# Kernel tuning notes

Hardware: AMD Instinct MI355X
Metric: run time of the kernel (lower is better)

## Reference

```python
import jax, jax.numpy as jnp
import numpy as np
import math

D_MODEL = 1024
N_HEADS = 16
RANK = 256  # int(d_model * 0.25)
RANK_PER_HEAD = RANK // N_HEADS  # 16
HEAD_DIM = D_MODEL // N_HEADS  # 64
B, L = 32, 512


def setup_inputs() -> dict:
    key = jax.random.key(0)
    kx, kq, kk, kv, ku, kvv = jax.random.split(key, 6)
    x = jax.random.normal(kx, (B, L, D_MODEL), dtype=jnp.float32)
    mask = jnp.ones((B, L), dtype=bool)
    s = 1.0 / math.sqrt(D_MODEL)
    Wq = jax.random.normal(kq, (RANK, D_MODEL), dtype=jnp.float32) * s
    Wk = jax.random.normal(kk, (RANK, D_MODEL), dtype=jnp.float32) * s
    Wv = jax.random.normal(kv, (RANK, D_MODEL), dtype=jnp.float32) * s
    # xavier_uniform for U [H, head_dim, r_h] and V [H, r_h, head_dim]
    lim = math.sqrt(6.0 / (HEAD_DIM + RANK_PER_HEAD))
    U = jax.random.uniform(ku, (N_HEADS, HEAD_DIM, RANK_PER_HEAD), jnp.float32, -lim, lim)
    V = jax.random.uniform(kvv, (N_HEADS, RANK_PER_HEAD, HEAD_DIM), jnp.float32, -lim, lim)
    return {"x": x, "mask": mask, "Wq": Wq, "Wk": Wk, "Wv": Wv, "U": U, "V": V}


def _rope_tables(seq_len, head_dim, dtype):
    half = head_dim // 2
    theta = 1.0 / (10000.0 ** (jnp.arange(half, dtype=jnp.float32) / half))
    freqs = jnp.arange(seq_len, dtype=jnp.float32)[:, None] * theta[None, :]  # [L, half]
    return jnp.cos(freqs).astype(dtype), jnp.sin(freqs).astype(dtype)


def _apply_rope(x, cos, sin):
    # x: [B, L, H, D]; complex multiply on interleaved pairs
    Bq, Lq, H, D = x.shape
    xr = x.reshape(Bq, Lq, H, D // 2, 2)
    x0, x1 = xr[..., 0], xr[..., 1]
    c = cos[None, :, None, :]
    s = sin[None, :, None, :]
    o0 = x0 * c - x1 * s
    o1 = x0 * s + x1 * c
    return jnp.stack([o0, o1], axis=-1).reshape(Bq, Lq, H, D)


def reference(x, mask, Wq, Wk, Wv, U, V):
    Bq, Lq, _ = x.shape
    H, head_dim, r_h = U.shape
    q_low = (x @ Wq.T).reshape(Bq, Lq, H, r_h)
    k_low = (x @ Wk.T).reshape(Bq, Lq, H, r_h)
    v_low = (x @ Wv.T).reshape(Bq, Lq, H, r_h)
    q = jnp.einsum('hdr,blhr->blhd', U, q_low)
    k = jnp.einsum('hdr,blhr->blhd', U, k_low)
    cos, sin = _rope_tables(Lq, head_dim, x.dtype)
    q = _apply_rope(q, cos, sin)
    k = _apply_rope(k, cos, sin)
    attn = jnp.einsum('blhd,bmhd->bhlm', q, k) / math.sqrt(head_dim)
    attn = jnp.where(mask[:, None, None, :], attn, -jnp.inf)
    attn = jax.nn.softmax(attn, axis=-1)
    out = jnp.einsum('bhlm,bmhr->blhr', attn, v_low)
    out = jnp.einsum('blhr,hrd->blhd', out, V)
    return out.reshape(Bq, Lq, H * head_dim)
```

## Files before the change

kernel.cpp:

```cpp
#include <hip/hip_runtime.h>
#include <hip/hip_bf16.h>

#define B_   32
#define L_   512
#define DM_  1024
#define H_   16
#define RH_  16
#define HD_  64
#define NTOK (B_ * L_)

typedef short s16x8 __attribute__((ext_vector_type(8)));
typedef float f32x4 __attribute__((ext_vector_type(4)));
#define MFMA16(a,b,c) __builtin_amdgcn_mfma_f32_16x16x32_bf16(a, b, c, 0, 0, 0)

#define GLOAD_LDS16(g, l) __builtin_amdgcn_global_load_lds( \
    (const __attribute__((address_space(1))) unsigned int*)(g), \
    (__attribute__((address_space(3))) unsigned int*)(l), 16, 0, 0)

#if __has_builtin(__builtin_amdgcn_exp2f)
#define EXP2N(x) __builtin_amdgcn_exp2f(x)
#else
#define EXP2N(x) __expf((x) * 0.69314718055994531f)
#endif

__device__ inline ushort f2bf(float f) {
    unsigned u = __builtin_bit_cast(unsigned, f);
    u += 0x7fffu + ((u >> 16) & 1u);
    return (ushort)(u >> 16);
}
__device__ inline float bf2f(ushort u) {
    return __builtin_bit_cast(float, (unsigned)u << 16);
}

__global__ __launch_bounds__(256) void cvt_w(const float* __restrict__ Wq,
                                             const float* __restrict__ Wk,
                                             const float* __restrict__ Wv,
                                             ushort* __restrict__ dst) {
    const size_t i = ((size_t)blockIdx.x * 256 + threadIdx.x) * 8;
    const size_t sz = 256 * 1024;
    const float* src = (i < sz) ? (Wq + i) : (i < 2 * sz) ? (Wk + i - sz)
                                                          : (Wv + i - 2 * sz);
    float4 a = *(const float4*)(src);
    float4 b = *(const float4*)(src + 4);
    ushort o[8] = {f2bf(a.x), f2bf(a.y), f2bf(a.z), f2bf(a.w),
                   f2bf(b.x), f2bf(b.y), f2bf(b.z), f2bf(b.w)};
    *(uint4*)(dst + i) = *(const uint4*)o;
}

__global__ __launch_bounds__(256) void proj_mfma(
    const float*  __restrict__ X,
    const ushort* __restrict__ Bm,
    float* __restrict__ C)
{
    const int gid = blockIdx.x;
    const int g48 = gid / 48;
    const int rr  = gid - g48 * 48;
    const int bn  = rr >> 3;
    const int bm  = g48 * 8 + (rr & 7);
    const int tid = threadIdx.x;
    const int lane = tid & 63;
    const int ln15 = lane & 15, quad = lane >> 4;
    const int w = tid >> 6, wy = w >> 1, wx = w & 1;

    __shared__ ushort As[128 * 64];
    __shared__ ushort Bs[2][128 * 64];

    const int srow = tid >> 3;
    const int gch  = (tid & 7) ^ (srow & 7);
    const float*  Ag = X  + ((size_t)(bm * 128 + srow)) * DM_ + gch * 8;
    const ushort* Bg = Bm + ((size_t)(bn * 128 + srow)) * DM_ + gch * 8;
    ushort* Al = As + tid * 8;

    f32x4 acc[4][4] = {};
    float4 pa0[4], pa1[4];

    #pragma unroll
    for (int i = 0; i < 4; ++i)
        GLOAD_LDS16(Bg + (size_t)(i * 32) * DM_, &Bs[0][tid * 8 + i * 2048]);
    __builtin_amdgcn_sched_barrier(0);
    #pragma unroll
    for (int i = 0; i < 4; ++i) {
        pa0[i] = *(const float4*)(Ag + (size_t)(i * 32) * DM_);
        pa1[i] = *(const float4*)(Ag + (size_t)(i * 32) * DM_ + 4);
    }

    for (int kt = 0; kt < DM_ / 64; ++kt) {
        const int cur = kt & 1;
        __builtin_amdgcn_sched_barrier(0);
        __builtin_amdgcn_s_barrier();
        __builtin_amdgcn_sched_barrier(0);

        #pragma unroll
        for (int i = 0; i < 4; ++i) {
            ushort o[8] = {f2bf(pa0[i].x), f2bf(pa0[i].y), f2bf(pa0[i].z), f2bf(pa0[i].w),
                           f2bf(pa1[i].x), f2bf(pa1[i].y), f2bf(pa1[i].z), f2bf(pa1[i].w)};
            *(uint4*)(Al + i * 2048) = *(const uint4*)o;
        }
        if (kt < DM_ / 64 - 1) {
            const size_t ko = (size_t)(kt + 1) * 64;
            ushort* Bln = &Bs[cur ^ 1][tid * 8];
            #pragma unroll
            for (int i = 0; i < 4; ++i)
                GLOAD_LDS16(Bg + (size_t)(i * 32) * DM_ + ko, Bln + i * 2048);
            __builtin_amdgcn_sched_barrier(0);
            #pragma unroll
            for (int i = 0; i < 4; ++i) {
                pa0[i] = *(const float4*)(Ag + (size_t)(i * 32) * DM_ + ko);
                pa1[i] = *(const float4*)(Ag + (size_t)(i * 32) * DM_ + ko + 4);
            }
        }
        asm volatile("s_waitcnt lgkmcnt(0)" ::: "memory");
        __builtin_amdgcn_sched_barrier(0);
        __builtin_amdgcn_s_barrier();
        __builtin_amdgcn_sched_barrier(0);

        const ushort* Bcur = Bs[cur];
        s16x8 Af[4][2], Bf[4][2];
        #pragma unroll
        for (int i = 0; i < 4; ++i) {
            const int m = wy * 64 + i * 16 + ln15;
            const int n = wx * 64 + i * 16 + ln15;
            #pragma unroll
            for (int kh = 0; kh < 2; ++kh) {
                const int c = kh * 4 + quad;
                Af[i][kh] = *(const s16x8*)&As[m * 64 + ((c ^ (m & 7)) * 8)];
                Bf[i][kh] = *(const s16x8*)&Bcur[n * 64 + ((c ^ (n & 7)) * 8)];
            }
        }
        #pragma unroll
        for (int i = 0; i < 4; ++i)
            #pragma unroll
            for (int j = 0; j < 4; ++j) {
                acc[i][j] = MFMA16(Af[i][0], Bf[j][0], acc[i][j]);
                acc[i][j] = MFMA16(Af[i][1], Bf[j][1], acc[i][j]);
            }
    }

    #pragma unroll
    for (int i = 0; i < 4; ++i) {
        #pragma unroll
        for (int r = 0; r < 4; ++r) {
            const int grow = bm * 128 + wy * 64 + i * 16 + quad * 4 + r;
            float* cp = C + (size_t)grow * 768 + bn * 128 + wx * 64 + ln15;
            #pragma unroll
            for (int j = 0; j < 4; ++j)
                cp[j * 16] = acc[i][j][r];
        }
    }
}

#define USTRIDE 1032
#define VSTRIDE 520

__global__ __launch_bounds__(512) void expand_rope(
    const float* __restrict__ low,
    const float* __restrict__ U,
    ushort* __restrict__ qr,
    ushort* __restrict__ kr,
    ushort* __restrict__ vt)
{
    const int blk = blockIdx.x;
    const int b   = blk >> 4;
    const int l0  = (blk & 15) * 32;
    const int tid = threadIdx.x;
    const int h   = tid >> 5;
    const int tok = tid & 31;
    const int l   = l0 + tok;
    const int t   = b * L_ + l;

    __shared__ ushort Uls[16 * USTRIDE];
    __shared__ ushort vst[16 * VSTRIDE];

    float ql[16], kl[16], vl[16];
    {
        const float* lp = low + (size_t)t * 768 + h * 16;
        #pragma unroll
        for (int j = 0; j < 4; ++j) {
            float4 a = *(const float4*)(lp + j * 4);
            float4 c = *(const float4*)(lp + 256 + j * 4);
            float4 v = *(const float4*)(lp + 512 + j * 4);
            ql[j*4+0]=a.x; ql[j*4+1]=a.y; ql[j*4+2]=a.z; ql[j*4+3]=a.w;
            kl[j*4+0]=c.x; kl[j*4+1]=c.y; kl[j*4+2]=c.z; kl[j*4+3]=c.w;
            vl[j*4+0]=v.x; vl[j*4+1]=v.y; vl[j*4+2]=v.z; vl[j*4+3]=v.w;
        }
    }

    #pragma unroll
    for (int k = 0; k < 8; ++k) {
        const int e4 = tid + k * 512;
        float4 u4 = ((const float4*)U)[e4];
        const int g = e4 * 4;
        const int hh = g >> 10, off = g & 1023;
        ushort o[4] = {f2bf(u4.x), f2bf(u4.y), f2bf(u4.z), f2bf(u4.w)};
        *(ushort4*)&Uls[hh * USTRIDE + off] = *(const ushort4*)o;
    }
    __syncthreads();

    #pragma unroll
    for (int r = 0; r < 16; ++r)
        vst[h * VSTRIDE + r * 32 + tok] = f2bf(vl[r]);

    const ushort* Uh = &Uls[h * USTRIDE];
    const size_t bh8 = (size_t)(b * H_ + h) * 8;
    ushort* qp = qr + (bh8 * L_ + (size_t)l) * 8;
    ushort* kp = kr + (bh8 * L_ + (size_t)l) * 8;
    const float L2C = 13.287712379549449f / 32.0f;
    const float QSCALE = 0.18033688011112042f;

    #pragma unroll
    for (int ch = 0; ch < 8; ++ch) {
        float qv[8], kv[8];
        #pragma unroll
        for (int d = 0; d < 8; ++d) {
            const int dd = ch * 8 + d;
            s16x8 u0 = *(const s16x8*)&Uh[dd * 16];
            s16x8 u1 = *(const s16x8*)&Uh[dd * 16 + 8];
            float s1 = 0.f, s2 = 0.f;
            #pragma unroll
            for (int r = 0; r < 8; ++r) {
                const float uf = bf2f((ushort)u0[r]);
                s1 = fmaf(uf, ql[r], s1);
                s2 = fmaf(uf, kl[r], s2);
            }
            #pragma unroll
            for (int r = 0; r < 8; ++r) {
                const float uf = bf2f((ushort)u1[r]);
                s1 = fmaf(uf, ql[8 + r], s1);
                s2 = fmaf(uf, kl[8 + r], s2);
            }
            qv[d] = s1; kv[d] = s2;
        }
        #pragma unroll
        for (int pj = 0; pj < 4; ++pj) {
            const int i = ch * 4 + pj;
            const float ang = (float)l * exp2f(-(float)i * L2C);
            const float c = __cosf(ang), s = __sinf(ang);
            float x0 = qv[2*pj], x1 = qv[2*pj+1];
            qv[2*pj]   = x0 * c - x1 * s;
            qv[2*pj+1] = x0 * s + x1 * c;
            x0 = kv[2*pj]; x1 = kv[2*pj+1];
            kv[2*pj]   = x0 * c - x1 * s;
            kv[2*pj+1] = x0 * s + x1 * c;
        }
        ushort qo[8], ko[8];
        #pragma unroll
        for (int d = 0; d < 8; ++d) {
            qo[d] = f2bf(qv[d] * QSCALE);
            ko[d] = f2bf(kv[d]);
        }
        *(uint4*)(qp + (size_t)ch * L_ * 8) = *(const uint4*)qo;
        *(uint4*)(kp + (size_t)ch * L_ * 8) = *(const uint4*)ko;
    }

    __syncthreads();

    #pragma unroll
    for (int k = 0; k < 2; ++k) {
        const int c = tid + k * 512;
        const int hh = c >> 6, rr = (c >> 2) & 15, j = c & 3;
        uint4 v = *(const uint4*)&vst[hh * VSTRIDE + rr * 32 + j * 8];
        *(uint4*)&vt[(((size_t)(b * H_ + hh) * RH_) + rr) * L_ + l0 + j * 8] = v;
    }
}

__global__ __launch_bounds__(512) void attn_mfma(
    const ushort* __restrict__ qr,
    const ushort* __restrict__ kr,
    const ushort* __restrict__ vt,
    const float*  __restrict__ V,
    float* __restrict__ out)
{
    const int gid = blockIdx.x;
    const int bh = ((gid >> 5) << 3) | (gid & 7);
    const int qt = (gid >> 3) & 3;
    const int b = bh >> 4, h = bh & 15;
    const int tid = threadIdx.x;
    const int w = tid >> 6, lane = tid & 63;
    const int ln15 = lane & 15, quad = lane >> 4;

    __shared__ ushort Ks[2][64 * 64];
    __shared__ ushort Vts[2][16 * 64];
    __shared__ ushort Pb[8][16 * 64];
    __shared__ float  VhS[16 * 64];

    if (tid < 256)
        *(float4*)&VhS[tid * 4] = *(const float4*)(V + (size_t)h * RH_ * HD_ + tid * 4);

    const int qrow = qt * 128 + w * 16 + ln15;
    const size_t bh8 = (size_t)bh * 8;
    s16x8 Qf0 = *(const s16x8*)(qr + ((bh8 + quad) * L_ + qrow) * 8);
    s16x8 Qf1 = *(const s16x8*)(qr + ((bh8 + 4 + quad) * L_ + qrow) * 8);

    const ushort* kbase = kr + bh8 * L_ * 8;
    const ushort* vbase = vt + (size_t)bh * RH_ * L_;

    float lsum = 0.f;
    f32x4 Oacc = {0.f, 0.f, 0.f, 0.f};

    auto stage = [&](int c, int buf) {
        {
            const int key = tid >> 3, ch = tid & 7;
            const int chS = ch ^ (key & 7);
            GLOAD_LDS16(kbase + ((size_t)chS * L_ + c * 64 + key) * 8,
                        &Ks[buf][tid * 8]);
        }
        if (w < 2) {
            const int r = tid >> 3, ch = tid & 7;
            GLOAD_LDS16(vbase + (size_t)r * L_ + c * 64 + ((ch ^ (r & 7)) * 8),
                        &Vts[buf][tid * 8]);
        }
    };

    stage(0, 0);
    __syncthreads();

    for (int c = 0; c < 8; ++c) {
        const int cur = c & 1;
        if (c < 7) stage(c + 1, cur ^ 1);

        f32x4 Sc[4];
        #pragma unroll
        for (int ct = 0; ct < 4; ++ct) {
            const int key = ln15 + 16 * ct;
            s16x8 k0 = *(const s16x8*)&Ks[cur][key * 64 + ((quad ^ (key & 7)) * 8)];
            s16x8 k1 = *(const s16x8*)&Ks[cur][key * 64 + (((4 + quad) ^ (key & 7)) * 8)];
            f32x4 acc = {0.f, 0.f, 0.f, 0.f};
            acc = MFMA16(k0, Qf0, acc);
            acc = MFMA16(k1, Qf1, acc);
            Sc[ct] = acc;
        }

        ushort* pb = Pb[w];
        float tsum = 0.f;
        #pragma unroll
        for (int ct = 0; ct < 4; ++ct) {
            const float p0 = EXP2N(Sc[ct][0]);
            const float p1 = EXP2N(Sc[ct][1]);
            const float p2 = EXP2N(Sc[ct][2]);
            const float p3 = EXP2N(Sc[ct][3]);
            tsum += (p0 + p1) + (p2 + p3);
            uint2 pk;
            pk.x = (unsigned)f2bf(p0) | ((unsigned)f2bf(p1) << 16);
            pk.y = (unsigned)f2bf(p2) | ((unsigned)f2bf(p3) << 16);
            const int key0 = ct * 16 + quad * 4;
            const int chp = key0 >> 3, kop = key0 & 7;
            *(uint2*)&pb[ln15 * 64 + ((chp ^ (ln15 & 7)) * 8) + kop] = pk;
        }
        lsum += tsum;

        asm volatile("s_waitcnt lgkmcnt(0)" ::: "memory");
        __builtin_amdgcn_sched_barrier(0);

        #pragma unroll
        for (int half = 0; half < 2; ++half) {
            const int ch = half * 4 + quad;
            s16x8 pa = *(const s16x8*)&pb[ln15 * 64 + ((ch ^ (ln15 & 7)) * 8)];
            s16x8 vb = *(const s16x8*)&Vts[cur][ln15 * 64 + ((ch ^ (ln15 & 7)) * 8)];
            Oacc = MFMA16(pa, vb, Oacc);
        }

        __syncthreads();
    }

    lsum += __shfl_xor(lsum, 16, 64);
    lsum += __shfl_xor(lsum, 32, 64);
    const float inv = 1.0f / lsum;

    float* Olds = (float*)Pb[w];
    #pragma unroll
    for (int r = 0; r < 4; ++r) {
        const float li = __shfl(inv, quad * 4 + r, 64);
        Olds[(quad * 4 + r) * 16 + ln15] = Oacc[r] * li;
    }
    asm volatile("s_waitcnt lgkmcnt(0)" ::: "memory");
    __builtin_amdgcn_sched_barrier(0);

    const int q = lane >> 2, dc = lane & 3;
    float orow[16];
    #pragma unroll
    for (int j = 0; j < 4; ++j) {
        float4 o4 = *(const float4*)&Olds[q * 16 + j * 4];
        orow[j * 4 + 0] = o4.x; orow[j * 4 + 1] = o4.y;
        orow[j * 4 + 2] = o4.z; orow[j * 4 + 3] = o4.w;
    }
    float4 res[4] = {};
    #pragma unroll
    for (int r = 0; r < 16; ++r) {
        const float ov = orow[r];
        #pragma unroll
        for (int j = 0; j < 4; ++j) {
            float4 v4 = *(const float4*)&VhS[r * 64 + dc * 16 + j * 4];
            res[j].x = fmaf(ov, v4.x, res[j].x);
            res[j].y = fmaf(ov, v4.y, res[j].y);
            res[j].z = fmaf(ov, v4.z, res[j].z);
            res[j].w = fmaf(ov, v4.w, res[j].w);
        }
    }
    const int l = qt * 128 + w * 16 + q;
    float* op = out + (((size_t)b * L_ + l) * H_ + h) * HD_ + dc * 16;
    #pragma unroll
    for (int j = 0; j < 4; ++j)
        *(float4*)(op + j * 4) = res[j];
}

extern "C" void kernel_launch(void* const* d_in, const int* in_sizes, int n_in,
                              void* d_out, int out_size, void* d_ws, size_t ws_size,
                              hipStream_t stream) {
    const float* x  = (const float*)d_in[0];
    const float* Wq = (const float*)d_in[2];
    const float* Wk = (const float*)d_in[3];
    const float* Wv = (const float*)d_in[4];
    const float* U  = (const float*)d_in[5];
    const float* V  = (const float*)d_in[6];
    float* out = (float*)d_out;

    float*  low = (float*)d_ws;
    ushort* Wb  = (ushort*)(low + (size_t)NTOK * 768);
    ushort* vtb = Wb + (size_t)768 * DM_;
    ushort* qrb = vtb + (size_t)B_ * H_ * RH_ * L_;
    ushort* krb = qrb + (size_t)B_ * H_ * L_ * HD_;

    cvt_w<<<768 * DM_ / (256 * 8), 256, 0, stream>>>(Wq, Wk, Wv, Wb);
    proj_mfma<<<768, 256, 0, stream>>>(x, Wb, low);
    expand_rope<<<512, 512, 0, stream>>>(low, U, qrb, krb, vtb);
    attn_mfma<<<B_ * H_ * 4, 512, 0, stream>>>(qrb, krb, vtb, V, out);
}
```

Measured before the change: 257.4 us.

## Split expand_rope work across head groups and output halves to raise occupancy

Restructures the expand_rope kernel from 512 blocks of 512 threads (one thread per token-head computing all 64 dims for q and k) into 2048 blocks of 256 threads. Each block now covers 4 heads, and each thread computes half the head dimensions, doing q and k one after the other. This cuts per-thread register pressure and shared-memory footprint (U staging is only 4 heads) and adds launch_bounds(256,5), aiming for more parallelism and better latency hiding. The cost is that each thread reloads its low-rank inputs and recomputes the rope angles, and the v transpose is done by half the threads.

```diff
diff --git a/kernel.cpp b/kernel.cpp
--- a/kernel.cpp
+++ b/kernel.cpp
@@ -149,10 +149,7 @@
     }
 }
 
-#define USTRIDE 1032
-#define VSTRIDE 520
-
-__global__ __launch_bounds__(512) void expand_rope(
+__global__ __launch_bounds__(256, 5) void expand_rope(
     const float* __restrict__ low,
     const float* __restrict__ U,
     ushort* __restrict__ qr,
@@ -160,106 +157,99 @@
     ushort* __restrict__ vt)
 {
     const int blk = blockIdx.x;
-    const int b   = blk >> 4;
-    const int l0  = (blk & 15) * 32;
+    const int b   = blk >> 6;
+    const int sub = blk & 63;
+    const int l0  = (sub >> 2) * 32;
+    const int hg  = sub & 3;
     const int tid = threadIdx.x;
-    const int h   = tid >> 5;
     const int tok = tid & 31;
+    const int h2  = (tid >> 5) & 3;
+    const int dh  = tid >> 7;
+    const int h   = hg * 4 + h2;
     const int l   = l0 + tok;
     const int t   = b * L_ + l;
 
-    __shared__ ushort Uls[16 * USTRIDE];
-    __shared__ ushort vst[16 * VSTRIDE];
-
-    float ql[16], kl[16], vl[16];
-    {
-        const float* lp = low + (size_t)t * 768 + h * 16;
-        #pragma unroll
-        for (int j = 0; j < 4; ++j) {
-            float4 a = *(const float4*)(lp + j * 4);
-            float4 c = *(const float4*)(lp + 256 + j * 4);
-            float4 v = *(const float4*)(lp + 512 + j * 4);
-            ql[j*4+0]=a.x; ql[j*4+1]=a.y; ql[j*4+2]=a.z; ql[j*4+3]=a.w;
-            kl[j*4+0]=c.x; kl[j*4+1]=c.y; kl[j*4+2]=c.z; kl[j*4+3]=c.w;
-            vl[j*4+0]=v.x; vl[j*4+1]=v.y; vl[j*4+2]=v.z; vl[j*4+3]=v.w;
-        }
-    }
-
-    #pragma unroll
-    for (int k = 0; k < 8; ++k) {
-        const int e4 = tid + k * 512;
-        float4 u4 = ((const float4*)U)[e4];
+    __shared__ ushort Uls[4 * 1032];
+    __shared__ ushort vst[4 * 520];
+
+    #pragma unroll
+    for (int k = 0; k < 4; ++k) {
+        const int e4 = tid + k * 256;
+        float4 u4 = ((const float4*)U)[(size_t)hg * 1024 + e4];
         const int g = e4 * 4;
         const int hh = g >> 10, off = g & 1023;
         ushort o[4] = {f2bf(u4.x), f2bf(u4.y), f2bf(u4.z), f2bf(u4.w)};
-        *(ushort4*)&Uls[hh * USTRIDE + off] = *(const ushort4*)o;
+        *(ushort4*)&Uls[hh * 1032 + off] = *(const ushort4*)o;
     }
     __syncthreads();
 
-    #pragma unroll
-    for (int r = 0; r < 16; ++r)
-        vst[h * VSTRIDE + r * 32 + tok] = f2bf(vl[r]);
-
-    const ushort* Uh = &Uls[h * USTRIDE];
-    const size_t bh8 = (size_t)(b * H_ + h) * 8;
-    ushort* qp = qr + (bh8 * L_ + (size_t)l) * 8;
-    ushort* kp = kr + (bh8 * L_ + (size_t)l) * 8;
     const float L2C = 13.287712379549449f / 32.0f;
     const float QSCALE = 0.18033688011112042f;
-
-    #pragma unroll
-    for (int ch = 0; ch < 8; ++ch) {
-        float qv[8], kv[8];
-        #pragma unroll
-        for (int d = 0; d < 8; ++d) {
-            const int dd = ch * 8 + d;
-            s16x8 u0 = *(const s16x8*)&Uh[dd * 16];
-            s16x8 u1 = *(const s16x8*)&Uh[dd * 16 + 8];
-            float s1 = 0.f, s2 = 0.f;
-            #pragma unroll
-            for (int r = 0; r < 8; ++r) {
-                const float uf = bf2f((ushort)u0[r]);
-                s1 = fmaf(uf, ql[r], s1);
-                s2 = fmaf(uf, kl[r], s2);
+    const float* lp = low + (size_t)t * 768 + h * 16;
+    const ushort* Uh = &Uls[h2 * 1032];
+
+    auto expand_store = [&](const float* src, float scale, ushort* dst) {
+        float in[16];
+        #pragma unroll
+        for (int j = 0; j < 4; ++j) {
+            float4 a = *(const float4*)(src + j * 4);
+            in[j*4+0] = a.x; in[j*4+1] = a.y; in[j*4+2] = a.z; in[j*4+3] = a.w;
+        }
+        #pragma unroll
+        for (int c2 = 0; c2 < 4; ++c2) {
+            const int ch = dh * 4 + c2;
+            float ov[8];
+            #pragma unroll
+            for (int d = 0; d < 8; ++d) {
+                const int dd = ch * 8 + d;
+                s16x8 u0 = *(const s16x8*)&Uh[dd * 16];
+                s16x8 u1 = *(const s16x8*)&Uh[dd * 16 + 8];
+                float s1 = 0.f;
+                #pragma unroll
+                for (int r = 0; r < 8; ++r)
+                    s1 = fmaf(bf2f((ushort)u0[r]), in[r], s1);
+                #pragma unroll
+                for (int r = 0; r < 8; ++r)
+                    s1 = fmaf(bf2f((ushort)u1[r]), in[8 + r], s1);
+                ov[d] = s1;
             }
             #pragma unroll
-            for (int r = 0; r < 8; ++r) {
-                const float uf = bf2f((ushort)u1[r]);
-                s1 = fmaf(uf, ql[8 + r], s1);
-                s2 = fmaf(uf, kl[8 + r], s2);
+            for (int pj = 0; pj < 4; ++pj) {
+                const int i = ch * 4 + pj;
+                const float ang = (float)l * exp2f(-(float)i * L2C);
+                const float cc = __cosf(ang), ss = __sinf(ang);
+                float x0 = ov[2*pj], x1 = ov[2*pj+1];
+                ov[2*pj]   = x0 * cc - x1 * ss;
+                ov[2*pj+1] = x0 * ss + x1 * cc;
             }
-            qv[d] = s1; kv[d] = s2;
-        }
-        #pragma unroll
-        for (int pj = 0; pj < 4; ++pj) {
-            const int i = ch * 4 + pj;
-            const float ang = (float)l * exp2f(-(float)i * L2C);
-            const float c = __cosf(ang), s = __sinf(ang);
-            float x0 = qv[2*pj], x1 = qv[2*pj+1];
-            qv[2*pj]   = x0 * c - x1 * s;
-            qv[2*pj+1] = x0 * s + x1 * c;
-            x0 = kv[2*pj]; x1 = kv[2*pj+1];
-            kv[2*pj]   = x0 * c - x1 * s;
-            kv[2*pj+1] = x0 * s + x1 * c;
-        }
-        ushort qo[8], ko[8];
-        #pragma unroll
-        for (int d = 0; d < 8; ++d) {
-            qo[d] = f2bf(qv[d] * QSCALE);
-            ko[d] = f2bf(kv[d]);
-        }
-        *(uint4*)(qp + (size_t)ch * L_ * 8) = *(const uint4*)qo;
-        *(uint4*)(kp + (size_t)ch * L_ * 8) = *(const uint4*)ko;
-    }
-
+            ushort o[8];
+            #pragma unroll
+            for (int d = 0; d < 8; ++d)
+                o[d] = f2bf(ov[d] * scale);
+            *(uint4*)(dst + (size_t)ch * L_ * 8) = *(const uint4*)o;
+        }
+    };
+
+    const size_t bh8 = (size_t)(b * H_ + h) * 8;
+    expand_store(lp,       QSCALE, qr + (bh8 * L_ + (size_t)l) * 8);
+    expand_store(lp + 256, 1.0f,   kr + (bh8 * L_ + (size_t)l) * 8);
+
+    if (dh == 0) {
+        #pragma unroll
+        for (int j = 0; j < 4; ++j) {
+            float4 v4 = *(const float4*)(lp + 512 + j * 4);
+            vst[h2 * 520 + (j*4+0) * 32 + tok] = f2bf(v4.x);
+            vst[h2 * 520 + (j*4+1) * 32 + tok] = f2bf(v4.y);
+            vst[h2 * 520 + (j*4+2) * 32 + tok] = f2bf(v4.z);
+            vst[h2 * 520 + (j*4+3) * 32 + tok] = f2bf(v4.w);
+        }
+    }
     __syncthreads();
 
-    #pragma unroll
-    for (int k = 0; k < 2; ++k) {
-        const int c = tid + k * 512;
-        const int hh = c >> 6, rr = (c >> 2) & 15, j = c & 3;
-        uint4 v = *(const uint4*)&vst[hh * VSTRIDE + rr * 32 + j * 8];
-        *(uint4*)&vt[(((size_t)(b * H_ + hh) * RH_) + rr) * L_ + l0 + j * 8] = v;
+    {
+        const int hh = tid >> 6, rr = (tid >> 2) & 15, j = tid & 3;
+        uint4 v = *(const uint4*)&vst[hh * 520 + rr * 32 + j * 8];
+        *(uint4*)&vt[(((size_t)(b * H_ + hg * 4 + hh) * RH_) + rr) * L_ + l0 + j * 8] = v;
     }
 }
 
@@ -422,6 +412,6 @@
 
     cvt_w<<<768 * DM_ / (256 * 8), 256, 0, stream>>>(Wq, Wk, Wv, Wb);
     proj_mfma<<<768, 256, 0, stream>>>(x, Wb, low);
-    expand_rope<<<512, 512, 0, stream>>>(low, U, qrb, krb, vtb);
+    expand_rope<<<2048, 256, 0, stream>>>(low, U, qrb, krb, vtb);
     attn_mfma<<<B_ * H_ * 4, 512, 0, stream>>>(qrb, krb, vtb, V, out);
 }
```

New measurement: 765.6 us. 2.97x slower.
